# Kernel optimization log

Hardware: AMD Instinct MI355X
Metric: run time of the kernel (lower is better)

## Reference

```python
import jax, jax.numpy as jnp
import numpy as np

B, S, D, H = 2, 2048, 1024, 16
HD = D // H  # 64


def setup_inputs() -> dict:
    key = jax.random.key(0)
    ks = jax.random.split(key, 6)
    x = jax.random.normal(ks[0], (B, S, D), dtype=jnp.float32)
    # rotary frequencies: theta = 10000^{-2i/hd}, angles = pos * theta
    inv_freq = 1.0 / (10000.0 ** (jnp.arange(0, HD, 2, dtype=jnp.float32) / HD))  # [HD/2]
    angles = jnp.arange(S, dtype=jnp.float32)[:, None] * inv_freq[None, :]  # [S, HD/2]
    freqs_cos = jnp.cos(angles)
    freqs_sin = jnp.sin(angles)
    scale = 0.02
    w_qkv = jax.random.normal(ks[1], (3 * D, D), dtype=jnp.float32) * scale
    b_qkv = jnp.zeros((3 * D,), dtype=jnp.float32)
    w_dense = jax.random.normal(ks[2], (D, D), dtype=jnp.float32) * scale
    b_dense = jnp.zeros((D,), dtype=jnp.float32)
    return {"x": x, "w_qkv": w_qkv, "b_qkv": b_qkv, "w_dense": w_dense,
            "b_dense": b_dense, "freqs_cos": freqs_cos, "freqs_sin": freqs_sin}


def _apply_rope(t, cos, sin):
    # t: [B, S, H, HD]; cos/sin: [S, HD/2] broadcast as [1, S, 1, HD/2]
    tr = t.reshape(t.shape[:-1] + (HD // 2, 2))
    x0, x1 = tr[..., 0], tr[..., 1]
    c = cos[None, :, None, :]
    s = sin[None, :, None, :]
    o0 = x0 * c - x1 * s  # real part of complex multiply
    o1 = x0 * s + x1 * c  # imag part
    return jnp.stack([o0, o1], axis=-1).reshape(t.shape)


def reference(x, w_qkv, b_qkv, w_dense, b_dense, freqs_cos, freqs_sin):
    b, s, d = x.shape
    qkv = x @ w_qkv.T + b_qkv              # [B, S, 3D]
    qkv = qkv.reshape(b, s, 3, H, HD)
    q, k, v = qkv[:, :, 0], qkv[:, :, 1], qkv[:, :, 2]  # [B, S, H, HD]
    q = _apply_rope(q, freqs_cos, freqs_sin)
    k = _apply_rope(k, freqs_cos, freqs_sin)
    # causal SDPA, scale = 1/sqrt(head_dim)
    q = q.transpose(0, 2, 1, 3)  # [B, H, S, HD]
    k = k.transpose(0, 2, 1, 3)
    v = v.transpose(0, 2, 1, 3)
    scores = jnp.einsum('bhqd,bhkd->bhqk', q, k) / jnp.sqrt(jnp.float32(HD))
    causal = jnp.tril(jnp.ones((s, s), dtype=bool))
    scores = jnp.where(causal[None, None], scores, jnp.finfo(scores.dtype).min)
    attn = jax.nn.softmax(scores, axis=-1)
    ctx = jnp.einsum('bhqk,bhkd->bhqd', attn, v)   # [B, H, S, HD]
    ctx = ctx.transpose(0, 2, 1, 3).reshape(b, s, d)
    return ctx @ w_dense.T + b_dense
```

## Files before the change

### kernel.cpp

```cpp
#include <hip/hip_runtime.h>
#include <stdint.h>

#define Bb 2
#define Ss 2048
#define Dd 1024
#define Hh 16
#define HDd 64

typedef float f32x4 __attribute__((ext_vector_type(4)));
typedef __bf16 bf16x8 __attribute__((ext_vector_type(8)));
typedef __bf16 bf16x2 __attribute__((ext_vector_type(2)));
typedef short s16x8 __attribute__((ext_vector_type(8)));

__device__ inline unsigned short f2bf(float f) {
  unsigned u = __builtin_bit_cast(unsigned, f);
  u += 0x7fffu + ((u >> 16) & 1u);
  return (unsigned short)(u >> 16);
}
__device__ inline float bf2f(unsigned short h) {
  unsigned u = ((unsigned)h) << 16;
  return __builtin_bit_cast(float, u);
}
__device__ inline unsigned pkcvt(float a, float b) {
  bf16x2 v;
  v[0] = (__bf16)a;
  v[1] = (__bf16)b;
  return __builtin_bit_cast(unsigned, v);
}
__device__ inline float ex2(float x) {
#if __has_builtin(__builtin_amdgcn_exp2f)
  return __builtin_amdgcn_exp2f(x);
#else
  float r;
  asm("v_exp_f32 %0, %1\n\ts_nop 1" : "=v"(r) : "v"(x));
  return r;
#endif
}
__device__ inline int swz(int row, int soff) {
  return (row << 6) + ((((soff >> 3) ^ (row & 7)) << 3) | (soff & 7));
}

#define GLDS(dst, src)                                                        \
  __builtin_amdgcn_global_load_lds(                                           \
      (const __attribute__((address_space(1))) void*)(src),                   \
      (__attribute__((address_space(3))) void*)(dst), 16, 0, 0)

__global__ void cast_all(const float* __restrict__ x, const float* __restrict__ wq,
                         const float* __restrict__ wd, unsigned short* __restrict__ dst) {
  int i = blockIdx.x * blockDim.x + threadIdx.x;
  float4 v;
  if (i < 1048576) v = ((const float4*)x)[i];
  else if (i < 1835008) v = ((const float4*)wq)[i - 1048576];
  else v = ((const float4*)wd)[i - 1835008];
  ushort4 o;
  o.x = f2bf(v.x); o.y = f2bf(v.y); o.z = f2bf(v.z); o.w = f2bf(v.w);
  ((ushort4*)dst)[i] = o;
}

__global__ __launch_bounds__(512, 2) void gemm_qkv(
    const unsigned short* __restrict__ A, const unsigned short* __restrict__ Bw,
    const float* __restrict__ bias, unsigned short* __restrict__ qkvout,
    unsigned short* __restrict__ vtout,
    const float* __restrict__ fc, const float* __restrict__ fs) {
  const int K = 1024, NT = 16;
  __shared__ __align__(16) unsigned short Ah[2][2][128 * 32];
  __shared__ __align__(16) unsigned short Bh[2][2][192 * 32];
  const int tid = threadIdx.x;
  const int w = tid >> 6, l = tid & 63;
  const int lg = l >> 4, lr = l & 15;
  const int wm = w >> 2, wn = w & 3;
  int id = blockIdx.y * gridDim.x + blockIdx.x;
  const int nwg = gridDim.x * gridDim.y;
  id = (id & 7) * (nwg >> 3) + (id >> 3);
  const int bx = id % gridDim.x, by = id / gridDim.x;
  const int mbase = by * 128, nbase = bx * 192;

  const unsigned short *as0, *bs0, *bs1, *bs2;
  {
    int r_ = tid >> 2, s_ = (tid & 3) ^ ((r_ >> 1) & 3);
    as0 = A + (size_t)(mbase + r_) * K + s_ * 8;
    bs0 = Bw + (size_t)(nbase + r_) * K + s_ * 8;
    int cb2 = 512 + tid;
    int h2 = cb2 >= 768;
    int cw2 = cb2 - h2 * 768;
    int r2 = cw2 >> 2, s2 = (cw2 & 3) ^ ((r2 >> 1) & 3);
    bs1 = Bw + (size_t)(nbase + r2) * K + h2 * 32 + s2 * 8;
    int cw3 = 256 + tid;
    int r3 = cw3 >> 2, s3 = (cw3 & 3) ^ ((r3 >> 1) & 3);
    bs2 = Bw + (size_t)(nbase + r3) * K + 32 + s3 * 8;
  }
#define STAGE(buf, k0)                                                        \
  GLDS(&Ah[buf][0][0] + tid * 8, as0 + (k0));                                 \
  GLDS(&Ah[buf][0][0] + 4096 + tid * 8, as0 + 32 + (k0));                     \
  GLDS(&Bh[buf][0][0] + tid * 8, bs0 + (k0));                                 \
  GLDS(&Bh[buf][0][0] + (512 + tid) * 8, bs1 + (k0));                         \
  GLDS(&Bh[buf][0][0] + (1024 + tid) * 8, bs2 + (k0));

  STAGE(0, 0);
  __syncthreads();

  f32x4 acc[4][3] = {};
  for (int t = 0; t < NT; ++t) {
    const int cur = t & 1;
    if (t + 1 < NT) { STAGE(cur ^ 1, (t + 1) * 64); }
#pragma unroll
    for (int h = 0; h < 2; ++h) {
      bf16x8 bfr[3], af[4];
#pragma unroll
      for (int ni = 0; ni < 3; ++ni) {
        int row = wn * 48 + ni * 16 + lr;
        bfr[ni] = *(const bf16x8*)(&Bh[cur][h][row * 32 + ((lg ^ ((row >> 1) & 3)) << 3)]);
      }
#pragma unroll
      for (int j = 0; j < 4; ++j) {
        int row = wm * 64 + j * 16 + lr;
        af[j] = *(const bf16x8*)(&Ah[cur][h][row * 32 + ((lg ^ ((row >> 1) & 3)) << 3)]);
      }
      __builtin_amdgcn_s_setprio(1);
#pragma unroll
      for (int j = 0; j < 4; ++j)
#pragma unroll
        for (int ni = 0; ni < 3; ++ni)
          acc[j][ni] = __builtin_amdgcn_mfma_f32_16x16x32_bf16(
              af[j], bfr[ni], acc[j][ni], 0, 0, 0);
      __builtin_amdgcn_s_setprio(0);
    }
    __syncthreads();
  }
#undef STAGE

#pragma unroll
  for (int mi = 0; mi < 4; ++mi)
#pragma unroll
    for (int ni = 0; ni < 3; ++ni) {
      int col = nbase + wn * 48 + ni * 16 + lr;
      float bi = bias[col];
      int row0 = mbase + wm * 64 + mi * 16 + lg * 4;
      float o4[4];
#pragma unroll
      for (int r = 0; r < 4; ++r) o4[r] = acc[mi][ni][r] + bi;
      int sect = col >> 10;
      int d = col & 63;
      int srow0 = row0 & 2047;
      if (sect < 2) {
        int p = d >> 1;
#pragma unroll
        for (int r = 0; r < 4; ++r) {
          float vp = __shfl_xor(o4[r], 1);
          float c = fc[(srow0 + r) * 32 + p];
          float s = fs[(srow0 + r) * 32 + p];
          float o = (d & 1) ? (vp * s + o4[r] * c) : (o4[r] * c - vp * s);
          qkvout[(size_t)(row0 + r) * 3072 + col] = f2bf(o);
        }
      } else {
        int bh = (row0 >> 11) * 16 + ((col >> 6) & 15);
        uint2 o;
        o.x = pkcvt(o4[0], o4[1]);
        o.y = pkcvt(o4[2], o4[3]);
        *(uint2*)&vtout[((size_t)(bh * 64 + d)) * 2048 + srow0] = o;
      }
    }
}

__global__ __launch_bounds__(256) void gemm_bt(
    const unsigned short* __restrict__ A, const unsigned short* __restrict__ Bw,
    const float* __restrict__ bias, float* __restrict__ Cout,
    int M, int N, int K) {
  __shared__ __align__(16) unsigned short As[128 * 32];
  __shared__ __align__(16) unsigned short Bs[128 * 32];
  const int tid = threadIdx.x;
  const int w = tid >> 6, l = tid & 63;
  const int lg = l >> 4, lr = l & 15;
  const int mbase = blockIdx.y * 128, nbase = blockIdx.x * 128;
  const int wr = w >> 1, wc = w & 1;
  f32x4 acc[4][4] = {};

  for (int k0 = 0; k0 < K; k0 += 32) {
#pragma unroll
    for (int r = 0; r < 2; ++r) {
      int c = r * 256 + w * 64 + l;
      int row = c >> 2, c8 = c & 3;
      GLDS(As + c * 8, A + (size_t)(mbase + row) * K + k0 + c8 * 8);
      GLDS(Bs + c * 8, Bw + (size_t)(nbase + row) * K + k0 + c8 * 8);
    }
    __syncthreads();
    bf16x8 af[4], bfr[4];
#pragma unroll
    for (int mi = 0; mi < 4; ++mi)
      af[mi] = *(const bf16x8*)(As + (wr * 64 + mi * 16 + lr) * 32 + lg * 8);
#pragma unroll
    for (int ni = 0; ni < 4; ++ni)
      bfr[ni] = *(const bf16x8*)(Bs + (wc * 64 + ni * 16 + lr) * 32 + lg * 8);
#pragma unroll
    for (int mi = 0; mi < 4; ++mi)
#pragma unroll
      for (int ni = 0; ni < 4; ++ni)
        acc[mi][ni] = __builtin_amdgcn_mfma_f32_16x16x32_bf16(
            af[mi], bfr[ni], acc[mi][ni], 0, 0, 0);
    __syncthreads();
  }

#pragma unroll
  for (int mi = 0; mi < 4; ++mi) {
#pragma unroll
    for (int ni = 0; ni < 4; ++ni) {
      int col = nbase + wc * 64 + ni * 16 + lr;
      float bi = bias[col];
#pragma unroll
      for (int r = 0; r < 4; ++r) {
        int row = mbase + wr * 64 + mi * 16 + lg * 4 + r;
        Cout[(size_t)row * N + col] = acc[mi][ni][r] + bi;
      }
    }
  }
}

__global__ __launch_bounds__(512, 4) void attn(
    const unsigned short* __restrict__ qkv, const unsigned short* __restrict__ vt,
    unsigned short* __restrict__ ctx) {
  __shared__ __align__(16) unsigned short Ks[2][64 * 64];
  __shared__ __align__(16) unsigned short Vs[2][64 * 64];
  __shared__ __align__(16) unsigned short Ps[8][16 * 64];
  int did = blockIdx.x;
  int x = did & 7, rest = did >> 3;
  int bh = x * 4 + (rest & 3);
  int qi = 31 - (rest >> 2);
  int b = bh >> 4, h = bh & 15;
  int qbase = qi * 64;
  int tid = threadIdx.x;
  int w = tid >> 6, l = tid & 63;
  int lg = l >> 4, lr = l & 15;
  int wq = w & 3, wk = w >> 2;

  bf16x8 qb[2];
#pragma unroll
  for (int kc = 0; kc < 2; ++kc) {
    s16x8 qr = *(const s16x8*)(qkv +
        (size_t)(b * Ss + qbase + wq * 16 + lr) * 3072 + h * 64 + kc * 32 + lg * 8);
    bf16x8 qs;
#pragma unroll
    for (int e = 0; e < 8; ++e)
      qs[e] = (__bf16)(bf2f((unsigned short)qr[e]) * 0.18033688f);
    qb[kc] = qs;
  }

  int tt = tid >> 8, rr = (tid >> 2) & 63, sc = (tid & 3) * 16;
  const unsigned short* kp =
      qkv + ((size_t)(b * Ss) + rr) * 3072 + 1024 + h * 64 + sc;
  const unsigned short* vp = vt + ((size_t)bh * 64 + rr) * 2048 + sc;

  int nkt = qi + 1;
  int nsup = (nkt + 1) >> 1;

  if (tt < nkt) {
    const unsigned short* gk = kp + (size_t)tt * 64 * 3072;
    const unsigned short* gv = vp + tt * 64;
    *(s16x8*)&Ks[tt][swz(rr, sc)]     = *(const s16x8*)gk;
    *(s16x8*)&Ks[tt][swz(rr, sc + 8)] = *(const s16x8*)(gk + 8);
    *(s16x8*)&Vs[tt][swz(rr, sc)]     = *(const s16x8*)gv;
    *(s16x8*)&Vs[tt][swz(rr, sc + 8)] = *(const s16x8*)(gv + 8);
  }
  s16x8 rk0, rk1, rv0, rv1;
  if (2 + tt < nkt) {
    const unsigned short* gk = kp + (size_t)(2 + tt) * 64 * 3072;
    const unsigned short* gv = vp + (2 + tt) * 64;
    rk0 = *(const s16x8*)gk;  rk1 = *(const s16x8*)(gk + 8);
    rv0 = *(const s16x8*)gv;  rv1 = *(const s16x8*)(gv + 8);
  }
  __syncthreads();

  f32x4 acc[4] = {};
  float mrow = -1e30f, lsum = 0.f;

  for (int j = 0; j < nsup; ++j) {
    int kt = 2 * j + wk;
    if (kt < nkt) {
      f32x4 st[4] = {};
      __builtin_amdgcn_s_setprio(1);
#pragma unroll
      for (int kc = 0; kc < 2; ++kc) {
#pragma unroll
        for (int ni = 0; ni < 4; ++ni) {
          bf16x8 ka = *(const bf16x8*)&Ks[wk][swz(ni * 16 + lr, kc * 32 + lg * 8)];
          st[ni] = __builtin_amdgcn_mfma_f32_16x16x32_bf16(ka, qb[kc], st[ni], 0, 0, 0);
        }
      }
      __builtin_amdgcn_s_setprio(0);

      float tm = -1e30f;
      if (kt == qi) {
        int rq = wq * 16 + lr;
#pragma unroll
        for (int ni = 0; ni < 4; ++ni)
#pragma unroll
          for (int r4 = 0; r4 < 4; ++r4) {
            float s = st[ni][r4];
            if (ni * 16 + lg * 4 + r4 > rq) s = -1e30f;
            st[ni][r4] = s;
            tm = fmaxf(tm, s);
          }
      } else {
#pragma unroll
        for (int ni = 0; ni < 4; ++ni)
#pragma unroll
          for (int r4 = 0; r4 < 4; ++r4) tm = fmaxf(tm, st[ni][r4]);
      }
      if (!__all(tm <= mrow + 8.0f)) {
        tm = fmaxf(tm, __shfl_xor(tm, 16));
        tm = fmaxf(tm, __shfl_xor(tm, 32));
        float mnew = fmaxf(mrow, tm);
        float alpha = ex2(mrow - mnew);
        lsum *= alpha;
#pragma unroll
        for (int nd = 0; nd < 4; ++nd)
#pragma unroll
          for (int r4 = 0; r4 < 4; ++r4) acc[nd][r4] *= alpha;
        mrow = mnew;
      }
      float sum = 0.f;
#pragma unroll
      for (int ni = 0; ni < 4; ++ni)
#pragma unroll
        for (int r4 = 0; r4 < 4; ++r4) {
          float pe = ex2(st[ni][r4] - mrow);
          st[ni][r4] = pe;
          sum += pe;
        }
      lsum += sum;
#pragma unroll
      for (int ni = 0; ni < 4; ++ni) {
        uint2 wv;
        wv.x = pkcvt(st[ni][0], st[ni][1]);
        wv.y = pkcvt(st[ni][2], st[ni][3]);
        *(uint2*)&Ps[w][swz(lr, ni * 16 + lg * 4)] = wv;
      }
      __builtin_amdgcn_s_setprio(1);
#pragma unroll
      for (int kc = 0; kc < 2; ++kc) {
        bf16x8 pbf = *(const bf16x8*)&Ps[w][swz(lr, kc * 32 + lg * 8)];
#pragma unroll
        for (int nd = 0; nd < 4; ++nd) {
          bf16x8 va = *(const bf16x8*)&Vs[wk][swz(nd * 16 + lr, kc * 32 + lg * 8)];
          acc[nd] = __builtin_amdgcn_mfma_f32_16x16x32_bf16(va, pbf, acc[nd], 0, 0, 0);
        }
      }
      __builtin_amdgcn_s_setprio(0);
    }

    if (j + 1 < nsup) {
      __syncthreads();
      int tw = 2 * (j + 1) + tt;
      if (tw < nkt) {
        *(s16x8*)&Ks[tt][swz(rr, sc)]     = rk0;
        *(s16x8*)&Ks[tt][swz(rr, sc + 8)] = rk1;
        *(s16x8*)&Vs[tt][swz(rr, sc)]     = rv0;
        *(s16x8*)&Vs[tt][swz(rr, sc + 8)] = rv1;
      }
      int tn = 2 * (j + 2) + tt;
      if (tn < nkt) {
        const unsigned short* gk = kp + (size_t)tn * 64 * 3072;
        const unsigned short* gv = vp + tn * 64;
        rk0 = *(const s16x8*)gk;  rk1 = *(const s16x8*)(gk + 8);
        rv0 = *(const s16x8*)gv;  rv1 = *(const s16x8*)(gv + 8);
      }
      __syncthreads();
    }
  }

  lsum += __shfl_xor(lsum, 16);
  lsum += __shfl_xor(lsum, 32);
  __syncthreads();
  float* accS = (float*)Vs;
  float* mlS  = (float*)Ks;
  if (wk == 1) {
    float* as = accS + (wq * 64 + l) * 16;
#pragma unroll
    for (int nd = 0; nd < 4; ++nd) *(f32x4*)(as + nd * 4) = acc[nd];
    mlS[(wq * 64 + l) * 2 + 0] = mrow;
    mlS[(wq * 64 + l) * 2 + 1] = lsum;
  }
  __syncthreads();
  if (wk == 0) {
    const float* as = accS + (wq * 64 + l) * 16;
    float m1 = mlS[(wq * 64 + l) * 2 + 0];
    float l1 = mlS[(wq * 64 + l) * 2 + 1];
    float M  = fmaxf(mrow, m1);
    float s0 = ex2(mrow - M), s1 = ex2(m1 - M);
    float inv = 1.0f / (lsum * s0 + l1 * s1);
    float f0 = s0 * inv, f1 = s1 * inv;
    int qg = qbase + wq * 16 + lr;
#pragma unroll
    for (int nd = 0; nd < 4; ++nd) {
      f32x4 a1 = *(const f32x4*)(as + nd * 4);
      uint2 o;
      o.x = pkcvt(acc[nd][0] * f0 + a1[0] * f1, acc[nd][1] * f0 + a1[1] * f1);
      o.y = pkcvt(acc[nd][2] * f0 + a1[2] * f1, acc[nd][3] * f0 + a1[3] * f1);
      *(uint2*)&ctx[((size_t)(b * Ss) + qg) * 1024 + h * 64 + nd * 16 + lg * 4] = o;
    }
  }
}

extern "C" void kernel_launch(void* const* d_in, const int* in_sizes, int n_in,
                              void* d_out, int out_size, void* d_ws, size_t ws_size,
                              hipStream_t stream) {
  const float* x       = (const float*)d_in[0];
  const float* w_qkv   = (const float*)d_in[1];
  const float* b_qkv   = (const float*)d_in[2];
  const float* w_dense = (const float*)d_in[3];
  const float* b_dense = (const float*)d_in[4];
  const float* fc      = (const float*)d_in[5];
  const float* fs      = (const float*)d_in[6];
  float* out = (float*)d_out;

  char* ws = (char*)d_ws;
  unsigned short* xb    = (unsigned short*)(ws);
  unsigned short* wqkvb = (unsigned short*)(ws + (8ull  << 20));
  unsigned short* wdb   = (unsigned short*)(ws + (14ull << 20));
  unsigned short* qkvb  = (unsigned short*)(ws + (16ull << 20));
  unsigned short* vt    = (unsigned short*)(ws + (40ull << 20));

  cast_all<<<8192, 256, 0, stream>>>(x, w_qkv, w_dense, xb);

  gemm_qkv<<<dim3(16, 32), 512, 0, stream>>>(xb, wqkvb, b_qkv, qkvb, vt, fc, fs);
  attn<<<1024, 512, 0, stream>>>(qkvb, vt, xb );
  gemm_bt<<<dim3(8, 32), 256, 0, stream>>>(xb, wdb, b_dense, out,
                                           4096, 1024, 1024);
}
```

Measured before the change: 108.1 us.

## Halve attention block to 4 waves, each handling 32 query rows with direct-to-LDS KV loads

The attention kernel now runs 256 threads per block. Each wave computes two 16-row query sub-tiles, so every K and V fragment read from LDS feeds two MFMAs. K/V staging switches from register prefetch plus LDS store to GLDS direct global-to-LDS copies with an XOR swizzle. These copies are issued after the barrier for the next tile pair, which drops the one-step register prefetch. The change roughly doubles accumulator registers per wave and lowers launch bounds occupancy from 4 to 3, trading parallelism and latency hiding for less LDS traffic.

```diff
diff --git a/kernel.cpp b/kernel.cpp
--- a/kernel.cpp
+++ b/kernel.cpp
@@ -215,12 +215,12 @@
   }
 }
 
-__global__ __launch_bounds__(512, 4) void attn(
+__global__ __launch_bounds__(256, 3) void attn(
     const unsigned short* __restrict__ qkv, const unsigned short* __restrict__ vt,
     unsigned short* __restrict__ ctx) {
   __shared__ __align__(16) unsigned short Ks[2][64 * 64];
   __shared__ __align__(16) unsigned short Vs[2][64 * 64];
-  __shared__ __align__(16) unsigned short Ps[8][16 * 64];
+  __shared__ __align__(16) unsigned short Ps[4][32 * 64];
   int did = blockIdx.x;
   int x = did & 7, rest = did >> 3;
   int bh = x * 4 + (rest & 3);
@@ -230,118 +230,140 @@
   int tid = threadIdx.x;
   int w = tid >> 6, l = tid & 63;
   int lg = l >> 4, lr = l & 15;
-  int wq = w & 3, wk = w >> 2;
-
-  bf16x8 qb[2];
-#pragma unroll
-  for (int kc = 0; kc < 2; ++kc) {
-    s16x8 qr = *(const s16x8*)(qkv +
-        (size_t)(b * Ss + qbase + wq * 16 + lr) * 3072 + h * 64 + kc * 32 + lg * 8);
-    bf16x8 qs;
-#pragma unroll
-    for (int e = 0; e < 8; ++e)
-      qs[e] = (__bf16)(bf2f((unsigned short)qr[e]) * 0.18033688f);
-    qb[kc] = qs;
-  }
-
-  int tt = tid >> 8, rr = (tid >> 2) & 63, sc = (tid & 3) * 16;
-  const unsigned short* kp =
-      qkv + ((size_t)(b * Ss) + rr) * 3072 + 1024 + h * 64 + sc;
-  const unsigned short* vp = vt + ((size_t)bh * 64 + rr) * 2048 + sc;
+  int wq = w & 1, wk = w >> 1;
+  int qw = wq * 32;
+
+  bf16x8 qb[2][2];
+#pragma unroll
+  for (int mi = 0; mi < 2; ++mi)
+#pragma unroll
+    for (int kc = 0; kc < 2; ++kc) {
+      s16x8 qr = *(const s16x8*)(qkv +
+          (size_t)(b * Ss + qbase + qw + mi * 16 + lr) * 3072 + h * 64 + kc * 32 + lg * 8);
+      bf16x8 qs;
+#pragma unroll
+      for (int e = 0; e < 8; ++e)
+        qs[e] = (__bf16)(bf2f((unsigned short)qr[e]) * 0.18033688f);
+      qb[mi][kc] = qs;
+    }
+
+  int c1 = tid, c2 = 256 + tid;
+  int r1 = c1 >> 3, s1 = ((c1 & 7) ^ (r1 & 7)) * 8;
+  int r2 = c2 >> 3, s2 = ((c2 & 7) ^ (r2 & 7)) * 8;
+  const unsigned short* kg1 = qkv + ((size_t)(b * Ss) + r1) * 3072 + 1024 + h * 64 + s1;
+  const unsigned short* kg2 = qkv + ((size_t)(b * Ss) + r2) * 3072 + 1024 + h * 64 + s2;
+  const unsigned short* vg1 = vt + ((size_t)bh * 64 + r1) * 2048 + s1;
+  const unsigned short* vg2 = vt + ((size_t)bh * 64 + r2) * 2048 + s2;
+#define STAGEKV(kt)                                                           \
+  {                                                                           \
+    int tt_ = (kt) & 1;                                                       \
+    GLDS(&Ks[tt_][0] + c1 * 8, kg1 + (size_t)(kt) * 64 * 3072);               \
+    GLDS(&Ks[tt_][0] + c2 * 8, kg2 + (size_t)(kt) * 64 * 3072);               \
+    GLDS(&Vs[tt_][0] + c1 * 8, vg1 + (kt) * 64);                              \
+    GLDS(&Vs[tt_][0] + c2 * 8, vg2 + (kt) * 64);                              \
+  }
 
   int nkt = qi + 1;
   int nsup = (nkt + 1) >> 1;
 
-  if (tt < nkt) {
-    const unsigned short* gk = kp + (size_t)tt * 64 * 3072;
-    const unsigned short* gv = vp + tt * 64;
-    *(s16x8*)&Ks[tt][swz(rr, sc)]     = *(const s16x8*)gk;
-    *(s16x8*)&Ks[tt][swz(rr, sc + 8)] = *(const s16x8*)(gk + 8);
-    *(s16x8*)&Vs[tt][swz(rr, sc)]     = *(const s16x8*)gv;
-    *(s16x8*)&Vs[tt][swz(rr, sc + 8)] = *(const s16x8*)(gv + 8);
-  }
-  s16x8 rk0, rk1, rv0, rv1;
-  if (2 + tt < nkt) {
-    const unsigned short* gk = kp + (size_t)(2 + tt) * 64 * 3072;
-    const unsigned short* gv = vp + (2 + tt) * 64;
-    rk0 = *(const s16x8*)gk;  rk1 = *(const s16x8*)(gk + 8);
-    rv0 = *(const s16x8*)gv;  rv1 = *(const s16x8*)(gv + 8);
-  }
+  STAGEKV(0);
+  if (1 < nkt) STAGEKV(1);
   __syncthreads();
 
-  f32x4 acc[4] = {};
-  float mrow = -1e30f, lsum = 0.f;
+  f32x4 acc[4][2] = {};
+  float mrow[2] = {-1e30f, -1e30f}, lsum[2] = {0.f, 0.f};
 
   for (int j = 0; j < nsup; ++j) {
     int kt = 2 * j + wk;
     if (kt < nkt) {
-      f32x4 st[4] = {};
+      f32x4 st[4][2] = {};
       __builtin_amdgcn_s_setprio(1);
 #pragma unroll
       for (int kc = 0; kc < 2; ++kc) {
 #pragma unroll
         for (int ni = 0; ni < 4; ++ni) {
           bf16x8 ka = *(const bf16x8*)&Ks[wk][swz(ni * 16 + lr, kc * 32 + lg * 8)];
-          st[ni] = __builtin_amdgcn_mfma_f32_16x16x32_bf16(ka, qb[kc], st[ni], 0, 0, 0);
+#pragma unroll
+          for (int mi = 0; mi < 2; ++mi)
+            st[ni][mi] = __builtin_amdgcn_mfma_f32_16x16x32_bf16(
+                ka, qb[mi][kc], st[ni][mi], 0, 0, 0);
         }
       }
       __builtin_amdgcn_s_setprio(0);
 
-      float tm = -1e30f;
+      float tm[2] = {-1e30f, -1e30f};
       if (kt == qi) {
-        int rq = wq * 16 + lr;
+#pragma unroll
+        for (int mi = 0; mi < 2; ++mi) {
+          int rq = qw + mi * 16 + lr;
+#pragma unroll
+          for (int ni = 0; ni < 4; ++ni)
+#pragma unroll
+            for (int r4 = 0; r4 < 4; ++r4) {
+              float s = st[ni][mi][r4];
+              if (ni * 16 + lg * 4 + r4 > rq) s = -1e30f;
+              st[ni][mi][r4] = s;
+              tm[mi] = fmaxf(tm[mi], s);
+            }
+        }
+      } else {
+#pragma unroll
+        for (int mi = 0; mi < 2; ++mi)
+#pragma unroll
+          for (int ni = 0; ni < 4; ++ni)
+#pragma unroll
+            for (int r4 = 0; r4 < 4; ++r4) tm[mi] = fmaxf(tm[mi], st[ni][mi][r4]);
+      }
+      bool ok = (tm[0] <= mrow[0] + 8.0f) && (tm[1] <= mrow[1] + 8.0f);
+      if (!__all(ok)) {
+#pragma unroll
+        for (int mi = 0; mi < 2; ++mi) {
+          float t = fmaxf(tm[mi], __shfl_xor(tm[mi], 16));
+          t = fmaxf(t, __shfl_xor(t, 32));
+          float mnew = fmaxf(mrow[mi], t);
+          float alpha = ex2(mrow[mi] - mnew);
+          lsum[mi] *= alpha;
+#pragma unroll
+          for (int nd = 0; nd < 4; ++nd)
+#pragma unroll
+            for (int r4 = 0; r4 < 4; ++r4) acc[nd][mi][r4] *= alpha;
+          mrow[mi] = mnew;
+        }
+      }
+#pragma unroll
+      for (int mi = 0; mi < 2; ++mi) {
+        float sum = 0.f;
 #pragma unroll
         for (int ni = 0; ni < 4; ++ni)
 #pragma unroll
           for (int r4 = 0; r4 < 4; ++r4) {
-            float s = st[ni][r4];
-            if (ni * 16 + lg * 4 + r4 > rq) s = -1e30f;
-            st[ni][r4] = s;
-            tm = fmaxf(tm, s);
+            float pe = ex2(st[ni][mi][r4] - mrow[mi]);
+            st[ni][mi][r4] = pe;
+            sum += pe;
           }
-      } else {
-#pragma unroll
-        for (int ni = 0; ni < 4; ++ni)
-#pragma unroll
-          for (int r4 = 0; r4 < 4; ++r4) tm = fmaxf(tm, st[ni][r4]);
-      }
-      if (!__all(tm <= mrow + 8.0f)) {
-        tm = fmaxf(tm, __shfl_xor(tm, 16));
-        tm = fmaxf(tm, __shfl_xor(tm, 32));
-        float mnew = fmaxf(mrow, tm);
-        float alpha = ex2(mrow - mnew);
-        lsum *= alpha;
-#pragma unroll
-        for (int nd = 0; nd < 4; ++nd)
-#pragma unroll
-          for (int r4 = 0; r4 < 4; ++r4) acc[nd][r4] *= alpha;
-        mrow = mnew;
-      }
-      float sum = 0.f;
-#pragma unroll
-      for (int ni = 0; ni < 4; ++ni)
-#pragma unroll
-        for (int r4 = 0; r4 < 4; ++r4) {
-          float pe = ex2(st[ni][r4] - mrow);
-          st[ni][r4] = pe;
-          sum += pe;
-        }
-      lsum += sum;
-#pragma unroll
-      for (int ni = 0; ni < 4; ++ni) {
-        uint2 wv;
-        wv.x = pkcvt(st[ni][0], st[ni][1]);
-        wv.y = pkcvt(st[ni][2], st[ni][3]);
-        *(uint2*)&Ps[w][swz(lr, ni * 16 + lg * 4)] = wv;
+        lsum[mi] += sum;
+#pragma unroll
+        for (int ni = 0; ni < 4; ++ni) {
+          uint2 wv;
+          wv.x = pkcvt(st[ni][mi][0], st[ni][mi][1]);
+          wv.y = pkcvt(st[ni][mi][2], st[ni][mi][3]);
+          *(uint2*)&Ps[w][swz(mi * 16 + lr, ni * 16 + lg * 4)] = wv;
+        }
       }
       __builtin_amdgcn_s_setprio(1);
 #pragma unroll
       for (int kc = 0; kc < 2; ++kc) {
-        bf16x8 pbf = *(const bf16x8*)&Ps[w][swz(lr, kc * 32 + lg * 8)];
+        bf16x8 pbf[2];
+#pragma unroll
+        for (int mi = 0; mi < 2; ++mi)
+          pbf[mi] = *(const bf16x8*)&Ps[w][swz(mi * 16 + lr, kc * 32 + lg * 8)];
 #pragma unroll
         for (int nd = 0; nd < 4; ++nd) {
           bf16x8 va = *(const bf16x8*)&Vs[wk][swz(nd * 16 + lr, kc * 32 + lg * 8)];
-          acc[nd] = __builtin_amdgcn_mfma_f32_16x16x32_bf16(va, pbf, acc[nd], 0, 0, 0);
+#pragma unroll
+          for (int mi = 0; mi < 2; ++mi)
+            acc[nd][mi] = __builtin_amdgcn_mfma_f32_16x16x32_bf16(
+                va, pbf[mi], acc[nd][mi], 0, 0, 0);
         }
       }
       __builtin_amdgcn_s_setprio(0);
@@ -349,53 +371,57 @@
 
     if (j + 1 < nsup) {
       __syncthreads();
-      int tw = 2 * (j + 1) + tt;
-      if (tw < nkt) {
-        *(s16x8*)&Ks[tt][swz(rr, sc)]     = rk0;
-        *(s16x8*)&Ks[tt][swz(rr, sc + 8)] = rk1;
-        *(s16x8*)&Vs[tt][swz(rr, sc)]     = rv0;
-        *(s16x8*)&Vs[tt][swz(rr, sc + 8)] = rv1;
-      }
-      int tn = 2 * (j + 2) + tt;
-      if (tn < nkt) {
-        const unsigned short* gk = kp + (size_t)tn * 64 * 3072;
-        const unsigned short* gv = vp + tn * 64;
-        rk0 = *(const s16x8*)gk;  rk1 = *(const s16x8*)(gk + 8);
-        rv0 = *(const s16x8*)gv;  rv1 = *(const s16x8*)(gv + 8);
-      }
+      int t0 = 2 * (j + 1), t1 = t0 + 1;
+      STAGEKV(t0);
+      if (t1 < nkt) STAGEKV(t1);
       __syncthreads();
     }
   }
-
-  lsum += __shfl_xor(lsum, 16);
-  lsum += __shfl_xor(lsum, 32);
+#undef STAGEKV
+
+#pragma unroll
+  for (int mi = 0; mi < 2; ++mi) {
+    lsum[mi] += __shfl_xor(lsum[mi], 16);
+    lsum[mi] += __shfl_xor(lsum[mi], 32);
+  }
   __syncthreads();
-  float* accS = (float*)Vs;
-  float* mlS  = (float*)Ks;
+  float* aS0 = (float*)Ks;
+  float* aS1 = (float*)Vs;
+  float* mlS = (float*)Ps;
   if (wk == 1) {
-    float* as = accS + (wq * 64 + l) * 16;
-#pragma unroll
-    for (int nd = 0; nd < 4; ++nd) *(f32x4*)(as + nd * 4) = acc[nd];
-    mlS[(wq * 64 + l) * 2 + 0] = mrow;
-    mlS[(wq * 64 + l) * 2 + 1] = lsum;
+    int base = (wq * 64 + l) * 16;
+#pragma unroll
+    for (int nd = 0; nd < 4; ++nd) {
+      *(f32x4*)(aS0 + base + nd * 4) = acc[nd][0];
+      *(f32x4*)(aS1 + base + nd * 4) = acc[nd][1];
+    }
+    int mb = (wq * 64 + l) * 4;
+    mlS[mb] = mrow[0]; mlS[mb + 1] = lsum[0];
+    mlS[mb + 2] = mrow[1]; mlS[mb + 3] = lsum[1];
   }
   __syncthreads();
   if (wk == 0) {
-    const float* as = accS + (wq * 64 + l) * 16;
-    float m1 = mlS[(wq * 64 + l) * 2 + 0];
-    float l1 = mlS[(wq * 64 + l) * 2 + 1];
-    float M  = fmaxf(mrow, m1);
-    float s0 = ex2(mrow - M), s1 = ex2(m1 - M);
-    float inv = 1.0f / (lsum * s0 + l1 * s1);
-    float f0 = s0 * inv, f1 = s1 * inv;
-    int qg = qbase + wq * 16 + lr;
-#pragma unroll
-    for (int nd = 0; nd < 4; ++nd) {
-      f32x4 a1 = *(const f32x4*)(as + nd * 4);
-      uint2 o;
-      o.x = pkcvt(acc[nd][0] * f0 + a1[0] * f1, acc[nd][1] * f0 + a1[1] * f1);
-      o.y = pkcvt(acc[nd][2] * f0 + a1[2] * f1, acc[nd][3] * f0 + a1[3] * f1);
-      *(uint2*)&ctx[((size_t)(b * Ss) + qg) * 1024 + h * 64 + nd * 16 + lg * 4] = o;
+    int base = (wq * 64 + l) * 16;
+    int mb = (wq * 64 + l) * 4;
+#pragma unroll
+    for (int mi = 0; mi < 2; ++mi) {
+      const float* as = (mi ? aS1 : aS0) + base;
+      float m1 = mlS[mb + mi * 2], l1 = mlS[mb + mi * 2 + 1];
+      float M = fmaxf(mrow[mi], m1);
+      float s0 = ex2(mrow[mi] - M), s1 = ex2(m1 - M);
+      float inv = 1.0f / (lsum[mi] * s0 + l1 * s1);
+      float f0 = s0 * inv, f1 = s1 * inv;
+      int qg = qbase + qw + mi * 16 + lr;
+#pragma unroll
+      for (int nd = 0; nd < 4; ++nd) {
+        f32x4 a1 = *(const f32x4*)(as + nd * 4);
+        uint2 o;
+        o.x = pkcvt(acc[nd][mi][0] * f0 + a1[0] * f1,
+                    acc[nd][mi][1] * f0 + a1[1] * f1);
+        o.y = pkcvt(acc[nd][mi][2] * f0 + a1[2] * f1,
+                    acc[nd][mi][3] * f0 + a1[3] * f1);
+        *(uint2*)&ctx[((size_t)(b * Ss) + qg) * 1024 + h * 64 + nd * 16 + lg * 4] = o;
+      }
     }
   }
 }
@@ -422,7 +448,7 @@
   cast_all<<<8192, 256, 0, stream>>>(x, w_qkv, w_dense, xb);
 
   gemm_qkv<<<dim3(16, 32), 512, 0, stream>>>(xb, wqkvb, b_qkv, qkvb, vt, fc, fs);
-  attn<<<1024, 512, 0, stream>>>(qkvb, vt, xb );
+  attn<<<1024, 256, 0, stream>>>(qkvb, vt, xb );
   gemm_bt<<<dim3(8, 32), 256, 0, stream>>>(xb, wdb, b_dense, out,
                                            4096, 1024, 1024);
 }
```

New measurement: 104.5 us. -3.3%, faster.
